# Optimization experiments

Hardware: AMD Instinct MI355X
Metric: run time of the kernel (lower is better)

The kernel has to match this reference:

```python
import jax, jax.numpy as jnp
import numpy as np

T, IN, H, OUT = 4096, 1024, 2048, 1024


def setup_inputs() -> dict:
    key = jax.random.key(0)
    ks = jax.random.split(key, 7)
    s_x = np.float32(np.sqrt(2.0 / (IN + H)))   # Wx init scale
    s_h = np.float32(np.sqrt(1.0 / H))          # Wh init scale
    s_y = np.float32(np.sqrt(2.0 / (H + OUT)))  # Wy init scale
    return {
        "x": jax.random.normal(ks[0], (T, IN), jnp.float32),
        "Wx_f": jax.random.normal(ks[1], (H, IN), jnp.float32) * s_x,
        "Wh_f": jax.random.normal(ks[2], (H, H), jnp.float32) * s_h,
        "bh_f": jnp.zeros((H,), jnp.float32),
        "Wx_b": jax.random.normal(ks[3], (H, IN), jnp.float32) * s_x,
        "Wh_b": jax.random.normal(ks[4], (H, H), jnp.float32) * s_h,
        "bh_b": jnp.zeros((H,), jnp.float32),
        "Wy_f": jax.random.normal(ks[5], (OUT, H), jnp.float32) * s_y,
        "Wy_b": jax.random.normal(ks[6], (OUT, H), jnp.float32) * s_y,
        "by": jnp.zeros((OUT,), jnp.float32),
    }


def reference(x, Wx_f, Wh_f, bh_f, Wx_b, Wh_b, bh_b, Wy_f, Wy_b, by):
    # Precompute input projections for all timesteps (batched GEMM): [T, H]
    xWf = x @ Wx_f.T + bh_f
    xWb = x @ Wx_b.T + bh_b
    h0 = jnp.zeros((Wh_f.shape[0],), x.dtype)

    def make_step(Wh):
        def step(h, xw):
            h = jnp.tanh(xw + h @ Wh.T)
            return h, h
        return step

    # Forward direction: h_t = tanh(Wx x_t + Wh h_{t-1} + bh)
    _, hf = jax.lax.scan(make_step(Wh_f), h0, xWf)
    # Backward direction: same recurrence scanned from t=T-1 down to 0;
    # reverse=True yields outputs stacked in original time order,
    # matching h_backward_hist[::-1] in the torch code.
    _, hb = jax.lax.scan(make_step(Wh_b), h0, xWb, reverse=True)

    # Output per timestep: Wy_f h_f + Wy_b h_b + by -> [T, OUT], flattened
    y = hf @ Wy_f.T + hb @ Wy_b.T + by
    return y.reshape(-1)
```

## Files before the change

### kernel.cpp

```cpp
#include <hip/hip_runtime.h>
#include <hip/hip_bf16.h>
#include <math.h>

#define T_N   4096
#define IN_N  1024
#define H_N   2048
#define OUT_N 1024

#define KD3  64
#define RPB3 32
#define RTH3 1024

#define XW_F_OFF 0ull
#define XW_B_OFF 33554432ull
#define HF_OFF   67108864ull
#define HB_OFF   100663296ull
#define PROG_OFF 134217728ull

__global__ __launch_bounds__(128) void init_prog_kernel(unsigned* __restrict__ p) {
  p[threadIdx.x] = 0u;
}

__global__ __launch_bounds__(256) void gemm_xw_kernel(
    const float* __restrict__ x,
    const float* __restrict__ Wxf, const float* __restrict__ bhf,
    const float* __restrict__ Wxb, const float* __restrict__ bhb,
    float* __restrict__ xwf, float* __restrict__ xwb)
{
  const int dir = blockIdx.z;
  const float* __restrict__ B    = dir ? Wxb : Wxf;
  const float* __restrict__ bias = dir ? bhb : bhf;
  float* __restrict__ C          = dir ? xwb : xwf;
  const int bm0 = blockIdx.y * 64;
  const int bn0 = blockIdx.x * 64;

  __shared__ float As[16][65];
  __shared__ float Bs[16][65];
  const int tid  = threadIdx.x;
  const int ty   = tid >> 4, tx = tid & 15;
  const int lrow = tid >> 2, lkq = (tid & 3) << 2;
  float acc[4][4] = {};

  for (int k0 = 0; k0 < IN_N; k0 += 16) {
    float4 a4 = *(const float4*)(x + (size_t)(bm0 + lrow) * IN_N + k0 + lkq);
    float4 b4 = *(const float4*)(B + (size_t)(bn0 + lrow) * IN_N + k0 + lkq);
    As[lkq + 0][lrow] = a4.x; As[lkq + 1][lrow] = a4.y;
    As[lkq + 2][lrow] = a4.z; As[lkq + 3][lrow] = a4.w;
    Bs[lkq + 0][lrow] = b4.x; Bs[lkq + 1][lrow] = b4.y;
    Bs[lkq + 2][lrow] = b4.z; Bs[lkq + 3][lrow] = b4.w;
    __syncthreads();
#pragma unroll
    for (int k = 0; k < 16; ++k) {
      float a[4], b[4];
#pragma unroll
      for (int i = 0; i < 4; ++i) a[i] = As[k][ty * 4 + i];
#pragma unroll
      for (int j = 0; j < 4; ++j) b[j] = Bs[k][tx * 4 + j];
#pragma unroll
      for (int i = 0; i < 4; ++i)
#pragma unroll
        for (int j = 0; j < 4; ++j) acc[i][j] = fmaf(a[i], b[j], acc[i][j]);
    }
    __syncthreads();
  }
#pragma unroll
  for (int i = 0; i < 4; ++i) {
    float4 v;
    v.x = acc[i][0] + bias[bn0 + tx * 4 + 0];
    v.y = acc[i][1] + bias[bn0 + tx * 4 + 1];
    v.z = acc[i][2] + bias[bn0 + tx * 4 + 2];
    v.w = acc[i][3] + bias[bn0 + tx * 4 + 3];
    *(float4*)(C + (size_t)(bm0 + ty * 4 + i) * H_N + bn0 + tx * 4) = v;
  }
}

__global__ __launch_bounds__(256) void gemm_out_kernel(
    const float* __restrict__ hf, const float* __restrict__ hb,
    const float* __restrict__ Wyf, const float* __restrict__ Wyb,
    const float* __restrict__ by, float* __restrict__ y)
{
  const int bm0 = blockIdx.y * 64;
  const int bn0 = blockIdx.x * 64;
  __shared__ float As[16][65];
  __shared__ float Bs[16][65];
  const int tid  = threadIdx.x;
  const int ty   = tid >> 4, tx = tid & 15;
  const int lrow = tid >> 2, lkq = (tid & 3) << 2;
  float acc[4][4] = {};

#pragma unroll 1
  for (int pass = 0; pass < 2; ++pass) {
    const float* __restrict__ A = pass ? hb : hf;
    const float* __restrict__ B = pass ? Wyb : Wyf;
    for (int k0 = 0; k0 < H_N; k0 += 16) {
      float4 a4 = *(const float4*)(A + (size_t)(bm0 + lrow) * H_N + k0 + lkq);
      float4 b4 = *(const float4*)(B + (size_t)(bn0 + lrow) * H_N + k0 + lkq);
      As[lkq + 0][lrow] = a4.x; As[lkq + 1][lrow] = a4.y;
      As[lkq + 2][lrow] = a4.z; As[lkq + 3][lrow] = a4.w;
      Bs[lkq + 0][lrow] = b4.x; Bs[lkq + 1][lrow] = b4.y;
      Bs[lkq + 2][lrow] = b4.z; Bs[lkq + 3][lrow] = b4.w;
      __syncthreads();
#pragma unroll
      for (int k = 0; k < 16; ++k) {
        float a[4], b[4];
#pragma unroll
        for (int i = 0; i < 4; ++i) a[i] = As[k][ty * 4 + i];
#pragma unroll
        for (int j = 0; j < 4; ++j) b[j] = Bs[k][tx * 4 + j];
#pragma unroll
        for (int i = 0; i < 4; ++i)
#pragma unroll
          for (int j = 0; j < 4; ++j) acc[i][j] = fmaf(a[i], b[j], acc[i][j]);
      }
      __syncthreads();
    }
  }
#pragma unroll
  for (int i = 0; i < 4; ++i) {
    float4 v;
    v.x = acc[i][0] + by[bn0 + tx * 4 + 0];
    v.y = acc[i][1] + by[bn0 + tx * 4 + 1];
    v.z = acc[i][2] + by[bn0 + tx * 4 + 2];
    v.w = acc[i][3] + by[bn0 + tx * 4 + 3];
    *(float4*)(y + (size_t)(bm0 + ty * 4 + i) * OUT_N + bn0 + tx * 4) = v;
  }
}

__global__ __launch_bounds__(RTH3, 4) void recurrent_kernel(
    const float* __restrict__ Whf, const float* __restrict__ Whb,
    const float* __restrict__ xwf, const float* __restrict__ xwb,
    float* __restrict__ hf, float* __restrict__ hb,
    unsigned* __restrict__ progf, unsigned* __restrict__ progb)
{
  const int b    = blockIdx.x;
  const bool fwd = (b < KD3);
  const int bb   = fwd ? b : b - KD3;
  const int rb   = bb * RPB3;
  const float* __restrict__ Wh = fwd ? Whf : Whb;
  const float* __restrict__ xw = fwd ? xwf : xwb;
  float* __restrict__ hist     = fwd ? hf : hb;
  unsigned* __restrict__ prog  = fwd ? progf : progb;

  const int w     = threadIdx.x >> 6;
  const int lane  = threadIdx.x & 63;
  const int jbase = lane << 2;
  const int r0    = rb + 2 * w;

  __shared__ __align__(16) float hs[H_N];

  float4 wv[2][8];
#pragma unroll
  for (int q = 0; q < 2; ++q)
#pragma unroll
    for (int k = 0; k < 8; ++k)
      wv[q][k] = *(const float4*)(Wh + (size_t)(r0 + q) * H_N + k * 256 + jbase);
#pragma unroll
  for (int q = 0; q < 2; ++q)
#pragma unroll
    for (int k = 0; k < 8; ++k)
      asm volatile("" : "+v"(wv[q][k].x), "+v"(wv[q][k].y),
                        "+v"(wv[q][k].z), "+v"(wv[q][k].w));

  for (int s = 0; s < T_N; ++s) {
    const int t  = fwd ? s : (T_N - 1 - s);
    const int pt = fwd ? (t - 1) : (t + 1);

    float xwv0 = 0.f, xwv1 = 0.f;
    if (lane == 0) {
      xwv0 = xw[(size_t)t * H_N + r0 + 0];
      xwv1 = xw[(size_t)t * H_N + r0 + 1];
    }

    if (s > 0) {
      if (w == 0) {
        for (;;) {
          unsigned p = __hip_atomic_load(prog + lane, __ATOMIC_RELAXED,
                                         __HIP_MEMORY_SCOPE_AGENT);
          if (__all(p >= (unsigned)s)) break;
          __builtin_amdgcn_s_sleep(1);
        }
        asm volatile("" ::: "memory");
      }
      __syncthreads();
      unsigned long long hv2 = __hip_atomic_load(
          (const unsigned long long*)(hist + (size_t)pt * H_N) + threadIdx.x,
          __ATOMIC_RELAXED, __HIP_MEMORY_SCOPE_AGENT);
      *((unsigned long long*)hs + threadIdx.x) = hv2;
      __syncthreads();
    } else {
      *((unsigned long long*)hs + threadIdx.x) = 0ull;
      __syncthreads();
    }

    float acc0 = 0.f, acc1 = 0.f;
#pragma unroll
    for (int k = 0; k < 8; ++k) {
      float4 h4 = *(const float4*)(hs + k * 256 + jbase);
      acc0 = fmaf(wv[0][k].x, h4.x, acc0);
      acc0 = fmaf(wv[0][k].y, h4.y, acc0);
      acc0 = fmaf(wv[0][k].z, h4.z, acc0);
      acc0 = fmaf(wv[0][k].w, h4.w, acc0);
      acc1 = fmaf(wv[1][k].x, h4.x, acc1);
      acc1 = fmaf(wv[1][k].y, h4.y, acc1);
      acc1 = fmaf(wv[1][k].z, h4.z, acc1);
      acc1 = fmaf(wv[1][k].w, h4.w, acc1);
    }
#pragma unroll
    for (int off = 32; off > 0; off >>= 1) {
      acc0 += __shfl_xor(acc0, off, 64);
      acc1 += __shfl_xor(acc1, off, 64);
    }

    if (lane == 0) {
      union { float f; unsigned u; } h0, h1;
      h0.f = tanhf(acc0 + xwv0);
      h1.f = tanhf(acc1 + xwv1);
      unsigned* hu = (unsigned*)(hist + (size_t)t * H_N + r0);
      __hip_atomic_store(hu + 0, h0.u, __ATOMIC_RELAXED, __HIP_MEMORY_SCOPE_AGENT);
      __hip_atomic_store(hu + 1, h1.u, __ATOMIC_RELAXED, __HIP_MEMORY_SCOPE_AGENT);
    }

    __syncthreads();
    if (threadIdx.x == 0)
      __hip_atomic_store(prog + bb, (unsigned)(s + 1), __ATOMIC_RELAXED,
                         __HIP_MEMORY_SCOPE_AGENT);
  }
}

extern "C" void kernel_launch(void* const* d_in, const int* in_sizes, int n_in,
                              void* d_out, int out_size, void* d_ws, size_t ws_size,
                              hipStream_t stream) {
  const float* x   = (const float*)d_in[0];
  const float* Wxf = (const float*)d_in[1];
  const float* Whf = (const float*)d_in[2];
  const float* bhf = (const float*)d_in[3];
  const float* Wxb = (const float*)d_in[4];
  const float* Whb = (const float*)d_in[5];
  const float* bhb = (const float*)d_in[6];
  const float* Wyf = (const float*)d_in[7];
  const float* Wyb = (const float*)d_in[8];
  const float* by  = (const float*)d_in[9];
  float* y = (float*)d_out;

  char* ws = (char*)d_ws;
  float* xwf      = (float*)(ws + XW_F_OFF);
  float* xwb      = (float*)(ws + XW_B_OFF);
  float* hf       = (float*)(ws + HF_OFF);
  float* hb       = (float*)(ws + HB_OFF);
  unsigned* progf = (unsigned*)(ws + PROG_OFF);
  unsigned* progb = progf + 64;

  hipLaunchKernelGGL(init_prog_kernel, dim3(1), dim3(128), 0, stream, progf);
  hipLaunchKernelGGL(gemm_xw_kernel, dim3(H_N / 64, T_N / 64, 2), dim3(256), 0, stream,
                     x, Wxf, bhf, Wxb, bhb, xwf, xwb);
  hipLaunchKernelGGL(recurrent_kernel, dim3(2 * KD3), dim3(RTH3), 0, stream,
                     Whf, Whb, xwf, xwb, hf, hb, progf, progb);
  hipLaunchKernelGGL(gemm_out_kernel, dim3(OUT_N / 64, T_N / 64), dim3(256), 0, stream,
                     hf, hb, Wyf, Wyb, by, y);
}
```

Baseline: 12.46 ms.

## Use bf16 MFMA for input and output projection GEMMs

Converts x and the projection weights to bf16 with a conversion kernel, then computes the input and output projections with 128x128-tiled MFMA bf16 GEMMs instead of scalar FP32 FMA tiles. The precomputed input projections are stored in bf16, halving the workspace and the per-step reads in the recurrence. The aim is to cut time spent in the two large GEMMs outside the sequential recurrence. The cost is reduced precision in the projections and extra conversion launches.

```diff
diff --git a/kernel.cpp b/kernel.cpp
--- a/kernel.cpp
+++ b/kernel.cpp
@@ -12,123 +12,174 @@
 #define RTH3 1024
 
 #define XW_F_OFF 0ull
-#define XW_B_OFF 33554432ull
-#define HF_OFF   67108864ull
-#define HB_OFF   100663296ull
-#define PROG_OFF 134217728ull
+#define XW_B_OFF 16777216ull
+#define HF_OFF   33554432ull
+#define HB_OFF   67108864ull
+#define XBF_OFF  100663296ull
+#define WXF_OFF  109051904ull
+#define WXB_OFF  113246208ull
+#define WYF_OFF  117440512ull
+#define WYB_OFF  121634816ull
+#define PROG_OFF 125829120ull
+
+typedef __attribute__((ext_vector_type(8))) short bf16x8;
+typedef __attribute__((ext_vector_type(4))) float f32x4;
+
+static __device__ __forceinline__ unsigned short f2bf(float f) {
+  unsigned x = __float_as_uint(f);
+  return (unsigned short)((x + 0x7FFFu + ((x >> 16) & 1u)) >> 16);
+}
+static __device__ __forceinline__ float bf2f(unsigned short u) {
+  return __uint_as_float(((unsigned)u) << 16);
+}
 
 __global__ __launch_bounds__(128) void init_prog_kernel(unsigned* __restrict__ p) {
   p[threadIdx.x] = 0u;
 }
 
-__global__ __launch_bounds__(256) void gemm_xw_kernel(
-    const float* __restrict__ x,
-    const float* __restrict__ Wxf, const float* __restrict__ bhf,
-    const float* __restrict__ Wxb, const float* __restrict__ bhb,
-    float* __restrict__ xwf, float* __restrict__ xwb)
+__global__ __launch_bounds__(256) void cvt_kernel(const float4* __restrict__ src,
+                                                  ushort4* __restrict__ dst, int n4) {
+  for (int i = blockIdx.x * 256 + threadIdx.x; i < n4; i += gridDim.x * 256) {
+    float4 v = src[i];
+    dst[i] = make_ushort4(f2bf(v.x), f2bf(v.y), f2bf(v.z), f2bf(v.w));
+  }
+}
+
+__global__ __launch_bounds__(256) void gemm_xw_mfma(
+    const unsigned short* __restrict__ xbf,
+    const unsigned short* __restrict__ Wf, const float* __restrict__ bhf,
+    const unsigned short* __restrict__ Wb, const float* __restrict__ bhb,
+    unsigned short* __restrict__ xwf, unsigned short* __restrict__ xwb)
 {
   const int dir = blockIdx.z;
-  const float* __restrict__ B    = dir ? Wxb : Wxf;
+  const unsigned short* __restrict__ W = dir ? Wb : Wf;
   const float* __restrict__ bias = dir ? bhb : bhf;
-  float* __restrict__ C          = dir ? xwb : xwf;
-  const int bm0 = blockIdx.y * 64;
-  const int bn0 = blockIdx.x * 64;
-
-  __shared__ float As[16][65];
-  __shared__ float Bs[16][65];
+  unsigned short* __restrict__ C = dir ? xwb : xwf;
+  const int bm0 = blockIdx.y * 128;
+  const int bn0 = blockIdx.x * 128;
+
+  __shared__ unsigned short As[128 * 40];
+  __shared__ unsigned short Bs[128 * 40];
+
   const int tid  = threadIdx.x;
-  const int ty   = tid >> 4, tx = tid & 15;
-  const int lrow = tid >> 2, lkq = (tid & 3) << 2;
-  float acc[4][4] = {};
-
-  for (int k0 = 0; k0 < IN_N; k0 += 16) {
-    float4 a4 = *(const float4*)(x + (size_t)(bm0 + lrow) * IN_N + k0 + lkq);
-    float4 b4 = *(const float4*)(B + (size_t)(bn0 + lrow) * IN_N + k0 + lkq);
-    As[lkq + 0][lrow] = a4.x; As[lkq + 1][lrow] = a4.y;
-    As[lkq + 2][lrow] = a4.z; As[lkq + 3][lrow] = a4.w;
-    Bs[lkq + 0][lrow] = b4.x; Bs[lkq + 1][lrow] = b4.y;
-    Bs[lkq + 2][lrow] = b4.z; Bs[lkq + 3][lrow] = b4.w;
+  const int w    = tid >> 6, lane = tid & 63;
+  const int wr   = w >> 1, wc = w & 1;
+  const int fr   = lane & 15, fc = lane >> 4;
+
+  f32x4 acc[4][4] = {};
+
+  for (int k0 = 0; k0 < IN_N; k0 += 32) {
+#pragma unroll
+    for (int i = 0; i < 2; ++i) {
+      int chunk = tid + i * 256;
+      int row = chunk >> 2, kk = (chunk & 3) * 8;
+      uint4 av = *(const uint4*)(xbf + (size_t)(bm0 + row) * IN_N + k0 + kk);
+      uint4 bv = *(const uint4*)(W   + (size_t)(bn0 + row) * IN_N + k0 + kk);
+      *(uint4*)(As + row * 40 + kk) = av;
+      *(uint4*)(Bs + row * 40 + kk) = bv;
+    }
     __syncthreads();
-#pragma unroll
-    for (int k = 0; k < 16; ++k) {
-      float a[4], b[4];
-#pragma unroll
-      for (int i = 0; i < 4; ++i) a[i] = As[k][ty * 4 + i];
-#pragma unroll
-      for (int j = 0; j < 4; ++j) b[j] = Bs[k][tx * 4 + j];
-#pragma unroll
-      for (int i = 0; i < 4; ++i)
-#pragma unroll
-        for (int j = 0; j < 4; ++j) acc[i][j] = fmaf(a[i], b[j], acc[i][j]);
-    }
+    bf16x8 af[4], bfr[4];
+#pragma unroll
+    for (int i = 0; i < 4; ++i)
+      af[i] = *(const bf16x8*)(As + (wr * 64 + i * 16 + fr) * 40 + fc * 8);
+#pragma unroll
+    for (int j = 0; j < 4; ++j)
+      bfr[j] = *(const bf16x8*)(Bs + (wc * 64 + j * 16 + fr) * 40 + fc * 8);
+#pragma unroll
+    for (int i = 0; i < 4; ++i)
+#pragma unroll
+      for (int j = 0; j < 4; ++j)
+        acc[i][j] = __builtin_amdgcn_mfma_f32_16x16x32_bf16(af[i], bfr[j],
+                                                            acc[i][j], 0, 0, 0);
     __syncthreads();
   }
 #pragma unroll
   for (int i = 0; i < 4; ++i) {
-    float4 v;
-    v.x = acc[i][0] + bias[bn0 + tx * 4 + 0];
-    v.y = acc[i][1] + bias[bn0 + tx * 4 + 1];
-    v.z = acc[i][2] + bias[bn0 + tx * 4 + 2];
-    v.w = acc[i][3] + bias[bn0 + tx * 4 + 3];
-    *(float4*)(C + (size_t)(bm0 + ty * 4 + i) * H_N + bn0 + tx * 4) = v;
-  }
-}
-
-__global__ __launch_bounds__(256) void gemm_out_kernel(
+    int row = bm0 + wr * 64 + i * 16 + fc * 4;
+#pragma unroll
+    for (int j = 0; j < 4; ++j) {
+      int col = bn0 + wc * 64 + j * 16 + fr;
+      float bv = bias[col];
+#pragma unroll
+      for (int q = 0; q < 4; ++q)
+        C[(size_t)(row + q) * H_N + col] = f2bf(acc[i][j][q] + bv);
+    }
+  }
+}
+
+__global__ __launch_bounds__(256) void gemm_out_mfma(
     const float* __restrict__ hf, const float* __restrict__ hb,
-    const float* __restrict__ Wyf, const float* __restrict__ Wyb,
+    const unsigned short* __restrict__ Wyf, const unsigned short* __restrict__ Wyb,
     const float* __restrict__ by, float* __restrict__ y)
 {
-  const int bm0 = blockIdx.y * 64;
-  const int bn0 = blockIdx.x * 64;
-  __shared__ float As[16][65];
-  __shared__ float Bs[16][65];
+  const int bm0 = blockIdx.y * 128;
+  const int bn0 = blockIdx.x * 128;
+
+  __shared__ unsigned short As[128 * 40];
+  __shared__ unsigned short Bs[128 * 40];
+
   const int tid  = threadIdx.x;
-  const int ty   = tid >> 4, tx = tid & 15;
-  const int lrow = tid >> 2, lkq = (tid & 3) << 2;
-  float acc[4][4] = {};
+  const int w    = tid >> 6, lane = tid & 63;
+  const int wr   = w >> 1, wc = w & 1;
+  const int fr   = lane & 15, fc = lane >> 4;
+
+  f32x4 acc[4][4] = {};
 
 #pragma unroll 1
   for (int pass = 0; pass < 2; ++pass) {
     const float* __restrict__ A = pass ? hb : hf;
-    const float* __restrict__ B = pass ? Wyb : Wyf;
-    for (int k0 = 0; k0 < H_N; k0 += 16) {
-      float4 a4 = *(const float4*)(A + (size_t)(bm0 + lrow) * H_N + k0 + lkq);
-      float4 b4 = *(const float4*)(B + (size_t)(bn0 + lrow) * H_N + k0 + lkq);
-      As[lkq + 0][lrow] = a4.x; As[lkq + 1][lrow] = a4.y;
-      As[lkq + 2][lrow] = a4.z; As[lkq + 3][lrow] = a4.w;
-      Bs[lkq + 0][lrow] = b4.x; Bs[lkq + 1][lrow] = b4.y;
-      Bs[lkq + 2][lrow] = b4.z; Bs[lkq + 3][lrow] = b4.w;
-      __syncthreads();
-#pragma unroll
-      for (int k = 0; k < 16; ++k) {
-        float a[4], b[4];
-#pragma unroll
-        for (int i = 0; i < 4; ++i) a[i] = As[k][ty * 4 + i];
-#pragma unroll
-        for (int j = 0; j < 4; ++j) b[j] = Bs[k][tx * 4 + j];
-#pragma unroll
-        for (int i = 0; i < 4; ++i)
-#pragma unroll
-          for (int j = 0; j < 4; ++j) acc[i][j] = fmaf(a[i], b[j], acc[i][j]);
+    const unsigned short* __restrict__ W = pass ? Wyb : Wyf;
+    for (int k0 = 0; k0 < H_N; k0 += 32) {
+#pragma unroll
+      for (int i = 0; i < 4; ++i) {
+        int chunk = tid + i * 256;
+        int row = chunk >> 3, c4 = chunk & 7;
+        float4 a4 = *(const float4*)(A + (size_t)(bm0 + row) * H_N + k0 + c4 * 4);
+        *(ushort4*)(As + row * 40 + c4 * 4) =
+            make_ushort4(f2bf(a4.x), f2bf(a4.y), f2bf(a4.z), f2bf(a4.w));
       }
+#pragma unroll
+      for (int i = 0; i < 2; ++i) {
+        int chunk = tid + i * 256;
+        int row = chunk >> 2, kk = (chunk & 3) * 8;
+        uint4 bv = *(const uint4*)(W + (size_t)(bn0 + row) * H_N + k0 + kk);
+        *(uint4*)(Bs + row * 40 + kk) = bv;
+      }
+      __syncthreads();
+      bf16x8 af[4], bfr[4];
+#pragma unroll
+      for (int i = 0; i < 4; ++i)
+        af[i] = *(const bf16x8*)(As + (wr * 64 + i * 16 + fr) * 40 + fc * 8);
+#pragma unroll
+      for (int j = 0; j < 4; ++j)
+        bfr[j] = *(const bf16x8*)(Bs + (wc * 64 + j * 16 + fr) * 40 + fc * 8);
+#pragma unroll
+      for (int i = 0; i < 4; ++i)
+#pragma unroll
+        for (int j = 0; j < 4; ++j)
+          acc[i][j] = __builtin_amdgcn_mfma_f32_16x16x32_bf16(af[i], bfr[j],
+                                                              acc[i][j], 0, 0, 0);
       __syncthreads();
     }
   }
 #pragma unroll
   for (int i = 0; i < 4; ++i) {
-    float4 v;
-    v.x = acc[i][0] + by[bn0 + tx * 4 + 0];
-    v.y = acc[i][1] + by[bn0 + tx * 4 + 1];
-    v.z = acc[i][2] + by[bn0 + tx * 4 + 2];
-    v.w = acc[i][3] + by[bn0 + tx * 4 + 3];
-    *(float4*)(y + (size_t)(bm0 + ty * 4 + i) * OUT_N + bn0 + tx * 4) = v;
+    int row = bm0 + wr * 64 + i * 16 + fc * 4;
+#pragma unroll
+    for (int j = 0; j < 4; ++j) {
+      int col = bn0 + wc * 64 + j * 16 + fr;
+      float bv = by[col];
+#pragma unroll
+      for (int q = 0; q < 4; ++q)
+        y[(size_t)(row + q) * OUT_N + col] = acc[i][j][q] + bv;
+    }
   }
 }
 
 __global__ __launch_bounds__(RTH3, 4) void recurrent_kernel(
     const float* __restrict__ Whf, const float* __restrict__ Whb,
-    const float* __restrict__ xwf, const float* __restrict__ xwb,
+    const unsigned short* __restrict__ xwf, const unsigned short* __restrict__ xwb,
     float* __restrict__ hf, float* __restrict__ hb,
     unsigned* __restrict__ progf, unsigned* __restrict__ progb)
 {
@@ -137,7 +188,7 @@
   const int bb   = fwd ? b : b - KD3;
   const int rb   = bb * RPB3;
   const float* __restrict__ Wh = fwd ? Whf : Whb;
-  const float* __restrict__ xw = fwd ? xwf : xwb;
+  const unsigned short* __restrict__ xw = fwd ? xwf : xwb;
   float* __restrict__ hist     = fwd ? hf : hb;
   unsigned* __restrict__ prog  = fwd ? progf : progb;
 
@@ -167,8 +218,9 @@
 
     float xwv0 = 0.f, xwv1 = 0.f;
     if (lane == 0) {
-      xwv0 = xw[(size_t)t * H_N + r0 + 0];
-      xwv1 = xw[(size_t)t * H_N + r0 + 1];
+      unsigned xq = *(const unsigned*)(xw + (size_t)t * H_N + r0);
+      xwv0 = bf2f((unsigned short)xq);
+      xwv1 = bf2f((unsigned short)(xq >> 16));
     }
 
     if (s > 0) {
@@ -243,18 +295,34 @@
   float* y = (float*)d_out;
 
   char* ws = (char*)d_ws;
-  float* xwf      = (float*)(ws + XW_F_OFF);
-  float* xwb      = (float*)(ws + XW_B_OFF);
-  float* hf       = (float*)(ws + HF_OFF);
-  float* hb       = (float*)(ws + HB_OFF);
+  unsigned short* xwf = (unsigned short*)(ws + XW_F_OFF);
+  unsigned short* xwb = (unsigned short*)(ws + XW_B_OFF);
+  float* hf  = (float*)(ws + HF_OFF);
+  float* hb  = (float*)(ws + HB_OFF);
+  unsigned short* xbf   = (unsigned short*)(ws + XBF_OFF);
+  unsigned short* wxfb  = (unsigned short*)(ws + WXF_OFF);
+  unsigned short* wxbb  = (unsigned short*)(ws + WXB_OFF);
+  unsigned short* wyfb  = (unsigned short*)(ws + WYF_OFF);
+  unsigned short* wybb  = (unsigned short*)(ws + WYB_OFF);
   unsigned* progf = (unsigned*)(ws + PROG_OFF);
   unsigned* progb = progf + 64;
 
   hipLaunchKernelGGL(init_prog_kernel, dim3(1), dim3(128), 0, stream, progf);
-  hipLaunchKernelGGL(gemm_xw_kernel, dim3(H_N / 64, T_N / 64, 2), dim3(256), 0, stream,
-                     x, Wxf, bhf, Wxb, bhb, xwf, xwb);
+  hipLaunchKernelGGL(cvt_kernel, dim3(1024), dim3(256), 0, stream,
+                     (const float4*)x,   (ushort4*)xbf,  (T_N * IN_N) / 4);
+  hipLaunchKernelGGL(cvt_kernel, dim3(512), dim3(256), 0, stream,
+                     (const float4*)Wxf, (ushort4*)wxfb, (H_N * IN_N) / 4);
+  hipLaunchKernelGGL(cvt_kernel, dim3(512), dim3(256), 0, stream,
+                     (const float4*)Wxb, (ushort4*)wxbb, (H_N * IN_N) / 4);
+  hipLaunchKernelGGL(cvt_kernel, dim3(512), dim3(256), 0, stream,
+                     (const float4*)Wyf, (ushort4*)wyfb, (OUT_N * H_N) / 4);
+  hipLaunchKernelGGL(cvt_kernel, dim3(512), dim3(256), 0, stream,
+                     (const float4*)Wyb, (ushort4*)wybb, (OUT_N * H_N) / 4);
+
+  hipLaunchKernelGGL(gemm_xw_mfma, dim3(H_N / 128, T_N / 128, 2), dim3(256), 0, stream,
+                     xbf, wxfb, bhf, wxbb, bhb, xwf, xwb);
   hipLaunchKernelGGL(recurrent_kernel, dim3(2 * KD3), dim3(RTH3), 0, stream,
                      Whf, Whb, xwf, xwb, hf, hb, progf, progb);
-  hipLaunchKernelGGL(gemm_out_kernel, dim3(OUT_N / 64, T_N / 64), dim3(256), 0, stream,
-                     hf, hb, Wyf, Wyb, by, y);
-}
+  hipLaunchKernelGGL(gemm_out_mfma, dim3(OUT_N / 128, T_N / 128), dim3(256), 0, stream,
+                     hf, hb, wyfb, wybb, by, y);
+}
```

Result: faster. 11.22 ms (-9.9%).
